# Kernel tuning notes

Measured on AMD Instinct MI355X. Metric: run time of the kernel, lower is better.

Reference implementation:

```python
import jax, jax.numpy as jnp
import numpy as np

N_HEADS = 4
D_K = 64
SCALE = D_K ** (-0.5)


def setup_inputs() -> dict:
    key = jax.random.key(0)
    k1, k2, k3, k4, k5 = jax.random.split(key, 5)
    B, C, H, W = 16, 256, 32, 32
    x = jax.random.normal(k1, (B, C, H, W), dtype=jnp.float32)
    # Linear weights stored as (in, out) for x @ W convention
    w_qkv = jax.random.normal(k2, (C, N_HEADS * D_K * 3), dtype=jnp.float32) * (C ** -0.5)
    b_qkv = jax.random.normal(k3, (N_HEADS * D_K * 3,), dtype=jnp.float32) * 0.02
    w_out = jax.random.normal(k4, (N_HEADS * D_K, C), dtype=jnp.float32) * ((N_HEADS * D_K) ** -0.5)
    b_out = jax.random.normal(k5, (C,), dtype=jnp.float32) * 0.02
    return {"x": x, "w_qkv": w_qkv, "b_qkv": b_qkv, "w_out": w_out, "b_out": b_out}


def reference(x, w_qkv, b_qkv, w_out, b_out):
    # NOTE: the original torch module defines GroupNorm but never applies it
    # in forward; we faithfully reproduce the forward as written.
    B, C, H, W = x.shape
    S = H * W
    xs = x.reshape(B, C, S).transpose(0, 2, 1)            # [B, S, C]
    qkv = (xs @ w_qkv + b_qkv).reshape(B, S, N_HEADS, 3 * D_K)
    q, k, v = jnp.split(qkv, 3, axis=-1)                   # each [B, S, H, d_k]
    attn = jnp.einsum('bihd,bjhd->bijh', q, k) * SCALE     # [B, S, S, H]
    attn = jax.nn.softmax(attn, axis=2)                    # softmax over j (keys)
    res = jnp.einsum('bijh,bjhd->bihd', attn, v)           # [B, S, H, d_k]
    res = res.reshape(B, S, N_HEADS * D_K)
    res = res @ w_out + b_out + xs                         # residual add
    return res.transpose(0, 2, 1).reshape(B, C, H, W)
```

## Files before the change

kernel.cpp:

```cpp
#include <hip/hip_runtime.h>
#include <hip/hip_bf16.h>

typedef __attribute__((ext_vector_type(8))) short short8;
typedef __attribute__((ext_vector_type(4))) short short4v;
typedef __attribute__((ext_vector_type(4))) float floatx4;
typedef unsigned short u16;

#define SCL_LOG2E 0.1803368801111204f

__device__ inline u16 f2b(float f) {
  __hip_bfloat16 h = __float2bfloat16(f);
  union { __hip_bfloat16 h; u16 u; } cv; cv.h = h; return cv.u;
}

__global__ __launch_bounds__(256) void tr64_f32_bf16(const float* __restrict__ in,
                                                     u16* __restrict__ out,
                                                     int R, int Cc) {
  __shared__ u16 tile[64][72];
  int bz = blockIdx.z;
  const float* inb = in + (size_t)bz * R * Cc;
  u16* outb = out + (size_t)bz * R * Cc;
  int c0 = blockIdx.x * 64, r0 = blockIdx.y * 64;
  int tx = threadIdx.x, ty = threadIdx.y;
#pragma unroll
  for (int i = 0; i < 4; i++) {
    int r = ty + 16 * i;
    float4 v = *(const float4*)&inb[(size_t)(r0 + r) * Cc + c0 + tx * 4];
    tile[tx * 4 + 0][r] = f2b(v.x);
    tile[tx * 4 + 1][r] = f2b(v.y);
    tile[tx * 4 + 2][r] = f2b(v.z);
    tile[tx * 4 + 3][r] = f2b(v.w);
  }
  __syncthreads();
#pragma unroll
  for (int i = 0; i < 4; i++) {
    int cc = ty + 16 * i;
    ushort4 o = *(ushort4*)&tile[cc][tx * 4];
    *(ushort4*)&outb[(size_t)(c0 + cc) * R + r0 + tx * 4] = o;
  }
}

__global__ __launch_bounds__(256) void qkv_gemm(const u16* __restrict__ xs,
                                                const float* __restrict__ wq,
                                                const float* __restrict__ bias,
                                                u16* __restrict__ Qo,
                                                u16* __restrict__ Ko,
                                                u16* __restrict__ Vto) {
  __shared__ u16 As[128 * 32];
  __shared__ u16 Bs[128 * 40];
  const int tid = threadIdx.x, wave = tid >> 6, lane = tid & 63;
  const int l15 = lane & 15, quad = lane >> 4;
  const int wm = (wave >> 1) * 64, wn = (wave & 1) * 64;
  const int m0 = blockIdx.x * 128, n0 = blockIdx.y * 128;
  const int bb = m0 >> 10, s0 = m0 & 1023;
  const int srow = wave * 32 + (lane >> 2), scol = (lane & 3) * 8;
  const int cl = tid >> 3, u = tid & 7;

  floatx4 acc[4][4] = {};

  for (int kt = 0; kt < 256; kt += 32) {
#pragma unroll
    for (int i = 0; i < 2; i++) {
      int r = srow + i * 16;
      *(short8*)&As[r * 32 + scol] =
          *(const short8*)&xs[((size_t)(bb * 1024 + s0 + r)) * 256 + kt + scol];
    }
    const float* wr = wq + (size_t)(kt + cl) * 768 + n0;
#pragma unroll
    for (int j = 0; j < 4; j++) {
      int e = u * 4 + 32 * j;
      float4 vb = *(const float4*)&wr[e];
      Bs[(e + 0) * 40 + cl] = f2b(vb.x);
      Bs[(e + 1) * 40 + cl] = f2b(vb.y);
      Bs[(e + 2) * 40 + cl] = f2b(vb.z);
      Bs[(e + 3) * 40 + cl] = f2b(vb.w);
    }
    __syncthreads();
    short8 af[4], bfr[4];
#pragma unroll
    for (int mi = 0; mi < 4; mi++)
      af[mi] = *(short8*)&As[(wm + mi * 16 + l15) * 32 + quad * 8];
#pragma unroll
    for (int ni = 0; ni < 4; ni++)
      bfr[ni] = *(short8*)&Bs[(wn + ni * 16 + l15) * 40 + quad * 8];
#pragma unroll
    for (int mi = 0; mi < 4; mi++)
#pragma unroll
      for (int ni = 0; ni < 4; ni++)
        acc[mi][ni] = __builtin_amdgcn_mfma_f32_16x16x32_bf16(af[mi], bfr[ni],
                                                              acc[mi][ni], 0, 0, 0);
    __syncthreads();
  }

#pragma unroll
  for (int ni = 0; ni < 4; ni++) {
    int n = n0 + wn + ni * 16 + l15;
    float bvv = bias[n];
    int h = n / 192;
    int rem = n - h * 192;
#pragma unroll
    for (int mi = 0; mi < 4; mi++) {
      int gm = m0 + wm + mi * 16 + quad * 4;
      int s = gm & 1023;
      if (rem < 128) {
        u16* dst;
        float scl;
        if (rem < 64) { dst = Qo; scl = SCL_LOG2E; } else { dst = Ko; scl = 1.0f; }
        int d = rem & 63;
#pragma unroll
        for (int r = 0; r < 4; r++)
          dst[((size_t)(bb * 4 + h) * 1024 + s + r) * 64 + d] =
              f2b((acc[mi][ni][r] + bvv) * scl);
      } else {
        int d = rem - 128;
        ushort4 pk;
        pk.x = f2b(acc[mi][ni][0] + bvv);
        pk.y = f2b(acc[mi][ni][1] + bvv);
        pk.z = f2b(acc[mi][ni][2] + bvv);
        pk.w = f2b(acc[mi][ni][3] + bvv);
        *(ushort4*)&Vto[((size_t)(bb * 4 + h) * 64 + d) * 1024 + s] = pk;
      }
    }
  }
}

__global__ __launch_bounds__(256, 2) void attn_kern(const u16* __restrict__ Q,
                                                    const u16* __restrict__ K,
                                                    const u16* __restrict__ Vt,
                                                    u16* __restrict__ O) {
  __shared__ u16 kv[2 * 2 * 64 * 72];
  const int bh = blockIdx.y;
  const u16* Qp = Q + (size_t)bh * 64 * 1024;
  const u16* Kp = K + (size_t)bh * 64 * 1024;
  const u16* Vp = Vt + (size_t)bh * 64 * 1024;
  u16* Op = O + (size_t)bh * 64 * 1024;
  const int q0 = blockIdx.x * 128;
  const int tid = threadIdx.x, wave = tid >> 6, lane = tid & 63;
  const int l15 = lane & 15, quad = lane >> 4;

  short8 qa[2][2];
#pragma unroll
  for (int qi = 0; qi < 2; qi++)
#pragma unroll
    for (int kh = 0; kh < 2; kh++)
      qa[qi][kh] = *(const short8*)&Qp[(size_t)(q0 + wave * 32 + qi * 16 + l15) * 64 +
                                       kh * 32 + quad * 8];

  const int srow = tid >> 2;
  const int sc = (tid & 3) * 16;

  {
    short8 k0 = *(const short8*)&Kp[(size_t)srow * 64 + sc];
    short8 k1 = *(const short8*)&Kp[(size_t)srow * 64 + sc + 8];
    short8 v0 = *(const short8*)&Vp[(size_t)srow * 1024 + sc];
    short8 v1 = *(const short8*)&Vp[(size_t)srow * 1024 + sc + 8];
    *(short8*)&kv[srow * 72 + sc] = k0;
    *(short8*)&kv[srow * 72 + sc + 8] = k1;
    *(short8*)&kv[4608 + srow * 72 + sc] = v0;
    *(short8*)&kv[4608 + srow * 72 + sc + 8] = v1;
  }
  __syncthreads();

  float lsum[2] = {0.f, 0.f};
  floatx4 acc[2][4] = {};

  for (int t = 0; t < 16; t++) {
    const u16* Ksb = kv + (t & 1) * 9216;
    const u16* Vsb = Ksb + 4608;

    short8 nk0, nk1, nv0, nv1;
    if (t < 15) {
      nk0 = *(const short8*)&Kp[(size_t)((t + 1) * 64 + srow) * 64 + sc];
      nk1 = *(const short8*)&Kp[(size_t)((t + 1) * 64 + srow) * 64 + sc + 8];
      nv0 = *(const short8*)&Vp[(size_t)srow * 1024 + (t + 1) * 64 + sc];
      nv1 = *(const short8*)&Vp[(size_t)srow * 1024 + (t + 1) * 64 + sc + 8];
    }

    short8 kb[4][2];
#pragma unroll
    for (int mj = 0; mj < 4; mj++)
#pragma unroll
      for (int kh = 0; kh < 2; kh++)
        kb[mj][kh] = *(const short8*)&Ksb[(mj * 16 + l15) * 72 + kh * 32 + quad * 8];

    floatx4 sf[2][4];
#pragma unroll
    for (int qi = 0; qi < 2; qi++)
#pragma unroll
      for (int mj = 0; mj < 4; mj++) {
        floatx4 z = {};
        z = __builtin_amdgcn_mfma_f32_16x16x32_bf16(kb[mj][0], qa[qi][0], z, 0, 0, 0);
        sf[qi][mj] =
            __builtin_amdgcn_mfma_f32_16x16x32_bf16(kb[mj][1], qa[qi][1], z, 0, 0, 0);
      }

    short4v pb[2][4];
#pragma unroll
    for (int qi = 0; qi < 2; qi++)
#pragma unroll
      for (int mj = 0; mj < 4; mj++) {
        float p0 = exp2f(sf[qi][mj][0]), p1 = exp2f(sf[qi][mj][1]);
        float p2 = exp2f(sf[qi][mj][2]), p3 = exp2f(sf[qi][mj][3]);
        lsum[qi] += (p0 + p1) + (p2 + p3);
        short4v pk;
        pk[0] = (short)f2b(p0); pk[1] = (short)f2b(p1);
        pk[2] = (short)f2b(p2); pk[3] = (short)f2b(p3);
        pb[qi][mj] = pk;
      }

#pragma unroll
    for (int c = 0; c < 4; c++)
#pragma unroll
      for (int md = 0; md < 4; md++) {
        short4v va = *(const short4v*)&Vsb[(md * 16 + l15) * 72 + c * 16 + quad * 4];
#pragma unroll
        for (int qi = 0; qi < 2; qi++)
          acc[qi][md] =
              __builtin_amdgcn_mfma_f32_16x16x16bf16_1k(va, pb[qi][c], acc[qi][md],
                                                        0, 0, 0);
      }

    if (t < 15) {
      u16* dst = kv + ((t + 1) & 1) * 9216;
      *(short8*)&dst[srow * 72 + sc] = nk0;
      *(short8*)&dst[srow * 72 + sc + 8] = nk1;
      *(short8*)&dst[4608 + srow * 72 + sc] = nv0;
      *(short8*)&dst[4608 + srow * 72 + sc + 8] = nv1;
    }
    __syncthreads();
  }

  float inv[2];
#pragma unroll
  for (int qi = 0; qi < 2; qi++) {
    lsum[qi] += __shfl_xor(lsum[qi], 16, 64);
    lsum[qi] += __shfl_xor(lsum[qi], 32, 64);
    inv[qi] = 1.f / lsum[qi];
  }

  __syncthreads();
  u16* Ot = kv;
#pragma unroll
  for (int qi = 0; qi < 2; qi++)
#pragma unroll
    for (int md = 0; md < 4; md++) {
      uint2 pk;
      u16 a0 = f2b(acc[qi][md][0] * inv[qi]), a1 = f2b(acc[qi][md][1] * inv[qi]);
      u16 a2 = f2b(acc[qi][md][2] * inv[qi]), a3 = f2b(acc[qi][md][3] * inv[qi]);
      pk.x = (unsigned)a0 | ((unsigned)a1 << 16);
      pk.y = (unsigned)a2 | ((unsigned)a3 << 16);
      *(uint2*)&Ot[(wave * 32 + qi * 16 + l15) * 72 + md * 16 + quad * 4] = pk;
    }
  __syncthreads();
#pragma unroll
  for (int rr = 0; rr < 4; rr++) {
    int row = wave * 32 + (lane >> 3) + 8 * rr;
    int col = (lane & 7) * 8;
    short8 v = *(const short8*)&Ot[row * 72 + col];
    *(short8*)&Op[(size_t)(q0 + row) * 64 + col] = v;
  }
}

__global__ __launch_bounds__(256) void out_gemm(const u16* __restrict__ Oin,
                                                const float* __restrict__ wo,
                                                const float* __restrict__ bias,
                                                const float* __restrict__ x,
                                                float* __restrict__ out) {
  __shared__ u16 As[64 * 32];
  __shared__ u16 Bs[128 * 40];
  const int tid = threadIdx.x, wave = tid >> 6, lane = tid & 63;
  const int l15 = lane & 15, quad = lane >> 4;
  const int wm = (wave >> 1) * 32, wn = (wave & 1) * 64;
  const int m0 = blockIdx.x * 64, n0 = blockIdx.y * 128;
  const int bb = m0 >> 10, s0 = m0 & 1023;
  const int ar = tid >> 2, ach = (tid & 3) * 8;
  const int cl = tid >> 3, u = tid & 7;

  floatx4 acc[2][4] = {};

  for (int kt = 0; kt < 256; kt += 32) {
    int h = kt >> 6, d0 = kt & 63;
    *(short8*)&As[ar * 32 + ach] =
        *(const short8*)&Oin[((size_t)(bb * 4 + h) * 1024 + s0 + ar) * 64 + d0 + ach];
    const float* wr = wo + (size_t)(kt + cl) * 256 + n0;
#pragma unroll
    for (int j = 0; j < 4; j++) {
      int e = u * 4 + 32 * j;
      float4 vb = *(const float4*)&wr[e];
      Bs[(e + 0) * 40 + cl] = f2b(vb.x);
      Bs[(e + 1) * 40 + cl] = f2b(vb.y);
      Bs[(e + 2) * 40 + cl] = f2b(vb.z);
      Bs[(e + 3) * 40 + cl] = f2b(vb.w);
    }
    __syncthreads();
    short8 af[2], bfr[4];
#pragma unroll
    for (int mi = 0; mi < 2; mi++)
      af[mi] = *(short8*)&As[(wm + mi * 16 + l15) * 32 + quad * 8];
#pragma unroll
    for (int ni = 0; ni < 4; ni++)
      bfr[ni] = *(short8*)&Bs[(wn + ni * 16 + l15) * 40 + quad * 8];
#pragma unroll
    for (int mi = 0; mi < 2; mi++)
#pragma unroll
      for (int ni = 0; ni < 4; ni++)
        acc[mi][ni] = __builtin_amdgcn_mfma_f32_16x16x32_bf16(af[mi], bfr[ni],
                                                              acc[mi][ni], 0, 0, 0);
    __syncthreads();
  }

#pragma unroll
  for (int ni = 0; ni < 4; ni++) {
    int c = n0 + wn + ni * 16 + l15;
    float bvv = bias[c];
#pragma unroll
    for (int mi = 0; mi < 2; mi++) {
      int gm = m0 + wm + mi * 16 + quad * 4;
      int s = gm & 1023;
      size_t idx = ((size_t)bb * 256 + c) * 1024 + s;
      float4 xr = *(const float4*)&x[idx];
      float4 o;
      o.x = acc[mi][ni][0] + bvv + xr.x;
      o.y = acc[mi][ni][1] + bvv + xr.y;
      o.z = acc[mi][ni][2] + bvv + xr.z;
      o.w = acc[mi][ni][3] + bvv + xr.w;
      *(float4*)&out[idx] = o;
    }
  }
}

extern "C" void kernel_launch(void* const* d_in, const int* in_sizes, int n_in,
                              void* d_out, int out_size, void* d_ws, size_t ws_size,
                              hipStream_t stream) {
  const float* x     = (const float*)d_in[0];
  const float* w_qkv = (const float*)d_in[1];
  const float* b_qkv = (const float*)d_in[2];
  const float* w_out = (const float*)d_in[3];
  const float* b_out = (const float*)d_in[4];
  float* out = (float*)d_out;
  char* ws = (char*)d_ws;

  u16* xs  = (u16*)(ws);
  u16* Qb  = (u16*)(ws + 8388608);
  u16* Kb  = (u16*)(ws + 16777216);
  u16* Vtb = (u16*)(ws + 25165824);
  u16* Ob  = xs;

  tr64_f32_bf16<<<dim3(16, 4, 16), dim3(16, 16), 0, stream>>>(x, xs, 256, 1024);
  qkv_gemm<<<dim3(128, 6), 256, 0, stream>>>(xs, w_qkv, b_qkv, Qb, Kb, Vtb);
  attn_kern<<<dim3(8, 64), 256, 0, stream>>>(Qb, Kb, Vtb, Ob);
  out_gemm<<<dim3(256, 2), 256, 0, stream>>>(Ob, w_out, b_out, x, out);
}
```

Measured before the change: 143.3 us.

## Triple-buffer K/V tiles in attention with two-ahead register prefetch; swap grid order

The attention kernel now uses three LDS buffers for K/V tiles and keeps a second tile in registers, so global loads run two iterations ahead instead of one. This is meant to hide more global memory latency behind the MFMA work. The grid is also transposed so consecutive blocks cover different batch-heads rather than different query tiles of the same head, which changes L2 sharing. LDS use grows by half, which could limit occupancy, and register pressure increases from the extra in-flight tile.

Measured after the change: 141.4 us. Within noise of the previous version (-1.3%).

```diff
diff --git a/kernel.cpp b/kernel.cpp
--- a/kernel.cpp
+++ b/kernel.cpp
@@ -128,13 +128,13 @@
                                                     const u16* __restrict__ K,
                                                     const u16* __restrict__ Vt,
                                                     u16* __restrict__ O) {
-  __shared__ u16 kv[2 * 2 * 64 * 72];
-  const int bh = blockIdx.y;
+  __shared__ u16 kv[3 * 2 * 64 * 72];
+  const int bh = blockIdx.x;
   const u16* Qp = Q + (size_t)bh * 64 * 1024;
   const u16* Kp = K + (size_t)bh * 64 * 1024;
   const u16* Vp = Vt + (size_t)bh * 64 * 1024;
   u16* Op = O + (size_t)bh * 64 * 1024;
-  const int q0 = blockIdx.x * 128;
+  const int q0 = blockIdx.y * 128;
   const int tid = threadIdx.x, wave = tid >> 6, lane = tid & 63;
   const int l15 = lane & 15, quad = lane >> 4;
 
@@ -148,32 +148,48 @@
 
   const int srow = tid >> 2;
   const int sc = (tid & 3) * 16;
-
-  {
-    short8 k0 = *(const short8*)&Kp[(size_t)srow * 64 + sc];
-    short8 k1 = *(const short8*)&Kp[(size_t)srow * 64 + sc + 8];
-    short8 v0 = *(const short8*)&Vp[(size_t)srow * 1024 + sc];
-    short8 v1 = *(const short8*)&Vp[(size_t)srow * 1024 + sc + 8];
-    *(short8*)&kv[srow * 72 + sc] = k0;
-    *(short8*)&kv[srow * 72 + sc + 8] = k1;
-    *(short8*)&kv[4608 + srow * 72 + sc] = v0;
-    *(short8*)&kv[4608 + srow * 72 + sc + 8] = v1;
-  }
+  const size_t kRow = (size_t)srow * 64 + sc;
+  const size_t vRow = (size_t)srow * 1024 + sc;
+
+  short8 t0k0 = *(const short8*)&Kp[kRow];
+  short8 t0k1 = *(const short8*)&Kp[kRow + 8];
+  short8 t0v0 = *(const short8*)&Vp[vRow];
+  short8 t0v1 = *(const short8*)&Vp[vRow + 8];
+  short8 t1k0 = *(const short8*)&Kp[kRow + 4096];
+  short8 t1k1 = *(const short8*)&Kp[kRow + 4096 + 8];
+  short8 t1v0 = *(const short8*)&Vp[vRow + 64];
+  short8 t1v1 = *(const short8*)&Vp[vRow + 64 + 8];
+  short8 r1k0 = *(const short8*)&Kp[kRow + 8192];
+  short8 r1k1 = *(const short8*)&Kp[kRow + 8192 + 8];
+  short8 r1v0 = *(const short8*)&Vp[vRow + 128];
+  short8 r1v1 = *(const short8*)&Vp[vRow + 128 + 8];
+  *(short8*)&kv[srow * 72 + sc] = t0k0;
+  *(short8*)&kv[srow * 72 + sc + 8] = t0k1;
+  *(short8*)&kv[4608 + srow * 72 + sc] = t0v0;
+  *(short8*)&kv[4608 + srow * 72 + sc + 8] = t0v1;
+  *(short8*)&kv[9216 + srow * 72 + sc] = t1k0;
+  *(short8*)&kv[9216 + srow * 72 + sc + 8] = t1k1;
+  *(short8*)&kv[9216 + 4608 + srow * 72 + sc] = t1v0;
+  *(short8*)&kv[9216 + 4608 + srow * 72 + sc + 8] = t1v1;
   __syncthreads();
 
   float lsum[2] = {0.f, 0.f};
   floatx4 acc[2][4] = {};
 
+  int cur = 0;
+  int wr = 2;
   for (int t = 0; t < 16; t++) {
-    const u16* Ksb = kv + (t & 1) * 9216;
+    const u16* Ksb = kv + cur * 9216;
     const u16* Vsb = Ksb + 4608;
 
-    short8 nk0, nk1, nv0, nv1;
-    if (t < 15) {
-      nk0 = *(const short8*)&Kp[(size_t)((t + 1) * 64 + srow) * 64 + sc];
-      nk1 = *(const short8*)&Kp[(size_t)((t + 1) * 64 + srow) * 64 + sc + 8];
-      nv0 = *(const short8*)&Vp[(size_t)srow * 1024 + (t + 1) * 64 + sc];
-      nv1 = *(const short8*)&Vp[(size_t)srow * 1024 + (t + 1) * 64 + sc + 8];
+    short8 r2k0, r2k1, r2v0, r2v1;
+    if (t < 13) {
+      size_t ko = kRow + (size_t)(t + 3) * 4096;
+      size_t vo = vRow + (size_t)(t + 3) * 64;
+      r2k0 = *(const short8*)&Kp[ko];
+      r2k1 = *(const short8*)&Kp[ko + 8];
+      r2v0 = *(const short8*)&Vp[vo];
+      r2v1 = *(const short8*)&Vp[vo + 8];
     }
 
     short8 kb[4][2];
@@ -220,13 +236,16 @@
                                                         0, 0, 0);
       }
 
-    if (t < 15) {
-      u16* dst = kv + ((t + 1) & 1) * 9216;
-      *(short8*)&dst[srow * 72 + sc] = nk0;
-      *(short8*)&dst[srow * 72 + sc + 8] = nk1;
-      *(short8*)&dst[4608 + srow * 72 + sc] = nv0;
-      *(short8*)&dst[4608 + srow * 72 + sc + 8] = nv1;
-    }
+    if (t < 14) {
+      u16* dst = kv + wr * 9216;
+      *(short8*)&dst[srow * 72 + sc] = r1k0;
+      *(short8*)&dst[srow * 72 + sc + 8] = r1k1;
+      *(short8*)&dst[4608 + srow * 72 + sc] = r1v0;
+      *(short8*)&dst[4608 + srow * 72 + sc + 8] = r1v1;
+    }
+    r1k0 = r2k0; r1k1 = r2k1; r1v0 = r2v0; r1v1 = r2v1;
+    cur = (cur == 2) ? 0 : cur + 1;
+    wr = (wr == 2) ? 0 : wr + 1;
     __syncthreads();
   }
 
@@ -238,7 +257,6 @@
     inv[qi] = 1.f / lsum[qi];
   }
 
-  __syncthreads();
   u16* Ot = kv;
 #pragma unroll
   for (int qi = 0; qi < 2; qi++)
@@ -348,6 +366,6 @@
 
   tr64_f32_bf16<<<dim3(16, 4, 16), dim3(16, 16), 0, stream>>>(x, xs, 256, 1024);
   qkv_gemm<<<dim3(128, 6), 256, 0, stream>>>(xs, w_qkv, b_qkv, Qb, Kb, Vtb);
-  attn_kern<<<dim3(8, 64), 256, 0, stream>>>(Qb, Kb, Vtb, Ob);
+  attn_kern<<<dim3(64, 8), 256, 0, stream>>>(Qb, Kb, Vtb, Ob);
   out_gemm<<<dim3(256, 2), 256, 0, stream>>>(Ob, w_out, b_out, x, out);
 }
```
